# Kernel optimization log

Hardware: AMD Instinct MI355X
Metric: run time of the kernel (lower is better)

Reference implementation:

```python
import jax, jax.numpy as jnp
import numpy as np

B, T, D, H, DK, FF, V, L = 2, 1024, 768, 12, 64, 3072, 50257, 12


def setup_inputs() -> dict:
    key = jax.random.key(0)
    ks = jax.random.split(key, 9)
    s = 0.02  # matches nn.init.normal_(std=0.02)
    rn = lambda k, sh: jax.random.normal(k, sh, jnp.float32) * s
    return {
        "x": jax.random.randint(ks[0], (B, T), 0, V),
        "tok_emb": rn(ks[1], (V, D)),
        "pos_emb": rn(ks[2], (T, D)),
        "Wq": rn(ks[3], (L, D, D)), "bq": jnp.zeros((L, D), jnp.float32),
        "Wk": rn(ks[4], (L, D, D)), "bk": jnp.zeros((L, D), jnp.float32),
        "Wv": rn(ks[5], (L, D, D)), "bv": jnp.zeros((L, D), jnp.float32),
        "Wo": rn(ks[6], (L, D, D)), "bo": jnp.zeros((L, D), jnp.float32),
        "ln1_g": jnp.ones((L, D), jnp.float32), "ln1_b": jnp.zeros((L, D), jnp.float32),
        "ln2_g": jnp.ones((L, D), jnp.float32), "ln2_b": jnp.zeros((L, D), jnp.float32),
        "W1": rn(ks[7], (L, D, FF)), "b1": jnp.zeros((L, FF), jnp.float32),
        "W2": rn(ks[8], (L, FF, D)), "b2": jnp.zeros((L, D), jnp.float32),
        "lnf_g": jnp.ones((D,), jnp.float32), "lnf_b": jnp.zeros((D,), jnp.float32),
    }


def _ln(x, g, b, eps=1e-5):
    m = jnp.mean(x, axis=-1, keepdims=True)
    v = jnp.var(x, axis=-1, keepdims=True)  # biased var, like torch LayerNorm
    return (x - m) * jax.lax.rsqrt(v + eps) * g + b


def _forward(x, tok_emb, pos_emb, Wq, bq, Wk, bk, Wv, bv, Wo, bo,
             ln1_g, ln1_b, ln2_g, ln2_b, W1, b1, W2, b2, lnf_g, lnf_b):
    Bsz, Tn = x.shape
    h = tok_emb[x] + pos_emb[:Tn][None]  # [B,T,D]
    causal = jnp.tril(jnp.ones((Tn, Tn), dtype=bool))  # True = keep
    scale = 1.0 / np.sqrt(DK)

    def block(h, p):
        wq, bq_, wk, bk_, wv, bv_, wo, bo_, g1, be1, g2, be2, w1, bf1, w2, bf2 = p
        x2 = _ln(h, g1, be1)
        q = (x2 @ wq + bq_).reshape(Bsz, Tn, H, DK)
        k = (x2 @ wk + bk_).reshape(Bsz, Tn, H, DK)
        v = (x2 @ wv + bv_).reshape(Bsz, Tn, H, DK)
        scores = jnp.einsum("bqhd,bkhd->bhqk", q, k) * scale
        scores = jnp.where(causal, scores, -jnp.inf)
        attn = jax.nn.softmax(scores, axis=-1)  # dropout is identity in eval
        ctx = jnp.einsum("bhqk,bkhd->bqhd", attn, v).reshape(Bsz, Tn, D)
        h = h + ctx @ wo + bo_
        x2 = _ln(h, g2, be2)
        ff = jax.nn.gelu(x2 @ w1 + bf1, approximate=False) @ w2 + bf2  # exact GELU like F.gelu
        return h + ff, None

    params = (Wq, bq, Wk, bk, Wv, bv, Wo, bo, ln1_g, ln1_b, ln2_g, ln2_b, W1, b1, W2, b2)
    h, _ = jax.lax.scan(block, h, params)
    h = _ln(h, lnf_g, lnf_b)
    return h @ tok_emb.T  # tied lm_head, [B,T,V]


def reference(x, tok_emb, pos_emb, Wq, bq, Wk, bk, Wv, bv, Wo, bo,
              ln1_g, ln1_b, ln2_g, ln2_b, W1, b1, W2, b2, lnf_g, lnf_b):
    return _forward(x, tok_emb, pos_emb, Wq, bq, Wk, bk, Wv, bv, Wo, bo,
                    ln1_g, ln1_b, ln2_g, ln2_b, W1, b1, W2, b2, lnf_g, lnf_b)
```

## Files before the change

kernel.cpp:

```cpp
#include <hip/hip_runtime.h>
#include <cmath>

#define DI __device__ __forceinline__

typedef unsigned short u16;
typedef __bf16 bf16x8 __attribute__((ext_vector_type(8)));
typedef float f32x4 __attribute__((ext_vector_type(4)));

static constexpr int Bsz = 2, T = 1024, D = 768, H = 12, FF = 3072, V = 50257, L = 12;
static constexpr int M = Bsz * T;

DI u16 f2bf(float f) {
  unsigned u = __float_as_uint(f);
  u = (u + 0x7fffu + ((u >> 16) & 1u)) >> 16;
  return (u16)u;
}
DI float bf2f(u16 h) { return __uint_as_float(((unsigned)h) << 16); }

DI void gload_lds16(const void* g, void* l) {
  __builtin_amdgcn_global_load_lds((const __attribute__((address_space(1))) void*)g,
                                   (__attribute__((address_space(3))) void*)l, 16, 0, 0);
}

__launch_bounds__(256)
__global__ void transpose_cvt(const float* __restrict__ src, u16* __restrict__ dst, int R, int C) {
  __shared__ float tile[32][33];
  const int tx = threadIdx.x, ty = threadIdx.y;
  const int c0 = blockIdx.x * 32, r0 = blockIdx.y * 32;
  src += (size_t)blockIdx.z * R * C;
  dst += (size_t)blockIdx.z * R * C;
#pragma unroll
  for (int i = 0; i < 4; ++i)
    tile[ty + i * 8][tx] = src[(size_t)(r0 + ty + i * 8) * C + c0 + tx];
  __syncthreads();
#pragma unroll
  for (int i = 0; i < 4; ++i)
    dst[(size_t)(c0 + ty + i * 8) * R + r0 + tx] = f2bf(tile[tx][ty + i * 8]);
}

__global__ void convert_bf16(const float* __restrict__ src, u16* __restrict__ dst, long n4) {
  long i = (long)blockIdx.x * blockDim.x + threadIdx.x;
  long stride = (long)gridDim.x * blockDim.x;
  for (; i < n4; i += stride) {
    float4 f = ((const float4*)src)[i];
    ushort4 o;
    o.x = f2bf(f.x); o.y = f2bf(f.y); o.z = f2bf(f.z); o.w = f2bf(f.w);
    ((ushort4*)dst)[i] = o;
  }
}

__launch_bounds__(256)
__global__ void embed_kernel(const int* __restrict__ x, const float* __restrict__ tok,
                             const float* __restrict__ pos, float* __restrict__ h) {
  const int row = blockIdx.x, t = threadIdx.x;
  const int tt = row % T;
  const int id = x[row];
  float* o = h + (size_t)row * D;
  const float* te = tok + (size_t)id * D;
  const float* pe = pos + (size_t)tt * D;
  o[t] = te[t] + pe[t];
  o[t + 256] = te[t + 256] + pe[t + 256];
  o[t + 512] = te[t + 512] + pe[t + 512];
}

__launch_bounds__(256)
__global__ void layernorm_kernel(const float* __restrict__ in, const float* __restrict__ gw,
                                 const float* __restrict__ bw, u16* __restrict__ out) {
  const int row = blockIdx.x, t = threadIdx.x;
  const int lane = t & 63, wid = t >> 6;
  const float* x = in + (size_t)row * D;
  float v0 = x[t], v1 = x[t + 256], v2 = x[t + 512];
  float sum = v0 + v1 + v2;
  float sq = v0 * v0 + v1 * v1 + v2 * v2;
  for (int off = 1; off < 64; off <<= 1) {
    sum += __shfl_xor(sum, off);
    sq += __shfl_xor(sq, off);
  }
  __shared__ float ps[4], pq[4];
  if (lane == 0) { ps[wid] = sum; pq[wid] = sq; }
  __syncthreads();
  sum = ps[0] + ps[1] + ps[2] + ps[3];
  sq = pq[0] + pq[1] + pq[2] + pq[3];
  const float mean = sum * (1.0f / D);
  const float var = sq * (1.0f / D) - mean * mean;
  const float rstd = rsqrtf(var + 1e-5f);
  u16* o = out + (size_t)row * D;
  o[t] = f2bf((v0 - mean) * rstd * gw[t] + bw[t]);
  o[t + 256] = f2bf((v1 - mean) * rstd * gw[t + 256] + bw[t + 256]);
  o[t + 512] = f2bf((v2 - mean) * rstd * gw[t + 512] + bw[t + 512]);
}

template <int EPI, int BM, int BN, int BK>
DI void gemm_core(const u16* __restrict__ A, const u16* __restrict__ Bt,
                  const float* bias, float* outF, u16* outH, const float* resid,
                  int N, int K, int m0, int n0) {
  __shared__ u16 sA[BM * BK];
  __shared__ u16 sB[BN * BK];
  constexpr int FM = BM / 32, FN = BN / 32;
  constexpr int CPR = BK / 8;
  constexpr int KS = BK / 32;
  constexpr int AI = BM * BK / 8 / 256;
  constexpr int BI = BN * BK / 8 / 256;
  const int t = threadIdx.x;
  const int lane = t & 63, wid = t >> 6;

  f32x4 acc[FM][FN] = {};
  const int wr = (wid >> 1) * (BM / 2), wc = (wid & 1) * (BN / 2);
  const int rsel = lane & 15, ksel = lane >> 4;

  for (int k0 = 0; k0 < K; k0 += BK) {
#pragma unroll
    for (int i = 0; i < AI; ++i) {
      int c = t + i * 256;
      int row = c / CPR, ch = c % CPR;
      int g = ch ^ (row & (CPR - 1));
      gload_lds16(A + (size_t)(m0 + row) * K + k0 + g * 8, &sA[c * 8]);
    }
#pragma unroll
    for (int i = 0; i < BI; ++i) {
      int c = t + i * 256;
      int row = c / CPR, ch = c % CPR;
      int g = ch ^ (row & (CPR - 1));
      int nr = n0 + row;
      if (nr >= N) nr = N - 1;
      gload_lds16(Bt + (size_t)nr * K + k0 + g * 8, &sB[c * 8]);
    }
    __syncthreads();
#pragma unroll
    for (int ks = 0; ks < KS; ++ks) {
      bf16x8 af[FM], bfr[FN];
#pragma unroll
      for (int m = 0; m < FM; ++m) {
        int row = wr + m * 16 + rsel;
        int ch = (ksel + 4 * ks) ^ (row & (CPR - 1));
        af[m] = *(const bf16x8*)&sA[row * BK + ch * 8];
      }
#pragma unroll
      for (int n = 0; n < FN; ++n) {
        int row = wc + n * 16 + rsel;
        int ch = (ksel + 4 * ks) ^ (row & (CPR - 1));
        bfr[n] = *(const bf16x8*)&sB[row * BK + ch * 8];
      }
#pragma unroll
      for (int m = 0; m < FM; ++m)
#pragma unroll
        for (int n = 0; n < FN; ++n)
          acc[m][n] = __builtin_amdgcn_mfma_f32_16x16x32_bf16(af[m], bfr[n], acc[m][n], 0, 0, 0);
    }
    __syncthreads();
  }

  const int rq = lane >> 4;
#pragma unroll
  for (int m = 0; m < FM; ++m) {
#pragma unroll
    for (int n = 0; n < FN; ++n) {
      const int col = n0 + wc + n * 16 + rsel;
      if (col >= N) continue;
      const float bv = bias ? bias[col] : 0.0f;
#pragma unroll
      for (int i = 0; i < 4; ++i) {
        const int row = m0 + wr + m * 16 + rq * 4 + i;
        float v = acc[m][n][i] + bv;
        const size_t idx = (size_t)row * N + col;
        if (EPI == 0) {
          outH[idx] = f2bf(v);
        } else if (EPI == 1) {
          float ge = 0.5f * v * (1.0f + erff(v * 0.70710678118f));
          outH[idx] = f2bf(ge);
        } else if (EPI == 2) {
          outF[idx] = resid[idx] + v;
        } else {
          outF[idx] = v;
        }
      }
    }
  }
}

__launch_bounds__(256) __global__ void gemm_qkv(const u16* __restrict__ A, const u16* __restrict__ Bt,
                                                const float* b0, const float* b1, const float* b2,
                                                u16* out, long zsB, long zsOut) {
  const int z = blockIdx.z;
  gemm_core<0, 128, 128, 64>(A, Bt + (size_t)z * zsB, z == 0 ? b0 : (z == 1 ? b1 : b2),
                             nullptr, out + (size_t)z * zsOut, nullptr, D, D,
                             blockIdx.x * 128, blockIdx.y * 128);
}
__launch_bounds__(256) __global__ void gemm_proj(const u16* __restrict__ A, const u16* __restrict__ Bt,
                                                 const float* bias, float* h) {
  gemm_core<2, 64, 64, 64>(A, Bt, bias, h, nullptr, h, D, D, blockIdx.x * 64, blockIdx.y * 64);
}
__launch_bounds__(256) __global__ void gemm_ff1(const u16* __restrict__ A, const u16* __restrict__ Bt,
                                                const float* bias, u16* out) {
  gemm_core<1, 128, 128, 64>(A, Bt, bias, nullptr, out, nullptr, FF, D,
                             blockIdx.x * 128, blockIdx.y * 128);
}
__launch_bounds__(256) __global__ void gemm_ff2(const u16* __restrict__ A, const u16* __restrict__ Bt,
                                                const float* bias, float* h) {
  gemm_core<2, 64, 64, 64>(A, Bt, bias, h, nullptr, h, D, FF, blockIdx.x * 64, blockIdx.y * 64);
}
__launch_bounds__(256) __global__ void gemm_lm(const u16* __restrict__ A, const u16* __restrict__ Bt,
                                               float* out) {
  const int flat = blockIdx.y * gridDim.x + blockIdx.x;
  const int nwg = gridDim.x * gridDim.y;
  const int cpx = nwg >> 3;
  const int nf = (flat & 7) * cpx + (flat >> 3);
  const int m0 = (nf & 15) * 128, n0 = (nf >> 4) * 128;
  gemm_core<3, 128, 128, 64>(A, Bt, nullptr, out, nullptr, nullptr, V, D, m0, n0);
}

__launch_bounds__(256)
__global__ void attn_mfma(const u16* __restrict__ qbuf, const u16* __restrict__ kbuf,
                          const u16* __restrict__ vbuf, u16* __restrict__ ctx) {
  __shared__ u16 sK[64 * 64];
  __shared__ u16 sVT[64 * 72];
  __shared__ u16 sP[4][16 * 72];
  const int t = threadIdx.x, lane = t & 63, wid = t >> 6;
  const int l15 = lane & 15, g = lane >> 4;
  const int qc = gridDim.x - 1 - blockIdx.x;
  const int q0 = qc * 64;
  const int bh = blockIdx.y;
  const int b = bh / H, hh = bh % H;
  const size_t rowbase = (size_t)b * T;
  u16* sPw = &sP[wid][0];

  const size_t qoff = (rowbase + q0 + wid * 16 + l15) * D + hh * 64 + g * 8;
  bf16x8 aQ0 = *(const bf16x8*)&qbuf[qoff];
  bf16x8 aQ1 = *(const bf16x8*)&qbuf[qoff + 32];
#pragma unroll
  for (int j = 0; j < 8; ++j) {
    aQ0[j] = (__bf16)(0.125f * (float)aQ0[j]);
    aQ1[j] = (__bf16)(0.125f * (float)aQ1[j]);
  }

  float mr[4] = {-INFINITY, -INFINITY, -INFINITY, -INFINITY};
  float lr[4] = {0.f, 0.f, 0.f, 0.f};
  f32x4 o[4] = {};
  const int nt = qc + 1;

  for (int kt = 0; kt < nt; ++kt) {
    __syncthreads();
#pragma unroll
    for (int i = 0; i < 2; ++i) {
      int c = t + i * 256;
      int row = c >> 3, ch = c & 7;
      gload_lds16(kbuf + (rowbase + kt * 64 + row) * D + hh * 64 + (size_t)(ch ^ (row & 7)) * 8,
                  &sK[c * 8]);
    }
#pragma unroll
    for (int i = 0; i < 2; ++i) {
      int key = t & 63, d0 = (t >> 6) * 8 + i * 32;
      bf16x8 v8 = *(const bf16x8*)&vbuf[(rowbase + kt * 64 + key) * D + hh * 64 + d0];
#pragma unroll
      for (int j = 0; j < 8; ++j) sVT[(d0 + j) * 72 + key] = ((u16*)&v8)[j];
    }
    __syncthreads();

    f32x4 s[4];
#pragma unroll
    for (int f = 0; f < 4; ++f) {
      const int krow = f * 16 + l15;
      bf16x8 bk0 = *(const bf16x8*)&sK[krow * 64 + ((g ^ (krow & 7)) * 8)];
      bf16x8 bk1 = *(const bf16x8*)&sK[krow * 64 + (((g + 4) ^ (krow & 7)) * 8)];
      f32x4 z = {};
      z = __builtin_amdgcn_mfma_f32_16x16x32_bf16(aQ0, bk0, z, 0, 0, 0);
      s[f] = __builtin_amdgcn_mfma_f32_16x16x32_bf16(aQ1, bk1, z, 0, 0, 0);
    }

    float p[4][4], scl[4];
    const bool diag = (kt == qc);
#pragma unroll
    for (int i = 0; i < 4; ++i) {
      float v0 = s[0][i], v1 = s[1][i], v2 = s[2][i], v3 = s[3][i];
      if (diag) {
        const int qrow = q0 + wid * 16 + g * 4 + i;
        const int kb = kt * 64 + l15;
        v0 = (kb <= qrow) ? v0 : -INFINITY;
        v1 = (kb + 16 <= qrow) ? v1 : -INFINITY;
        v2 = (kb + 32 <= qrow) ? v2 : -INFINITY;
        v3 = (kb + 48 <= qrow) ? v3 : -INFINITY;
      }
      float mt = fmaxf(fmaxf(v0, v1), fmaxf(v2, v3));
#pragma unroll
      for (int off = 1; off < 16; off <<= 1) mt = fmaxf(mt, __shfl_xor(mt, off));
      const float mn = fmaxf(mr[i], mt);
      const float sc = __expf(mr[i] - mn);
      p[0][i] = __expf(v0 - mn); p[1][i] = __expf(v1 - mn);
      p[2][i] = __expf(v2 - mn); p[3][i] = __expf(v3 - mn);
      float rs = p[0][i] + p[1][i] + p[2][i] + p[3][i];
#pragma unroll
      for (int off = 1; off < 16; off <<= 1) rs += __shfl_xor(rs, off);
      lr[i] = lr[i] * sc + rs;
      mr[i] = mn;
      scl[i] = sc;
    }
#pragma unroll
    for (int n = 0; n < 4; ++n) {
      o[n][0] *= scl[0]; o[n][1] *= scl[1]; o[n][2] *= scl[2]; o[n][3] *= scl[3];
    }
#pragma unroll
    for (int f = 0; f < 4; ++f)
#pragma unroll
      for (int i = 0; i < 4; ++i)
        sPw[(g * 4 + i) * 72 + f * 16 + l15] = f2bf(p[f][i]);

#pragma unroll
    for (int kb = 0; kb < 2; ++kb) {
      bf16x8 pa = *(const bf16x8*)&sPw[l15 * 72 + kb * 32 + g * 8];
#pragma unroll
      for (int n = 0; n < 4; ++n) {
        bf16x8 bv = *(const bf16x8*)&sVT[(n * 16 + l15) * 72 + kb * 32 + g * 8];
        o[n] = __builtin_amdgcn_mfma_f32_16x16x32_bf16(pa, bv, o[n], 0, 0, 0);
      }
    }
  }

  float inv[4] = {1.0f / lr[0], 1.0f / lr[1], 1.0f / lr[2], 1.0f / lr[3]};
#pragma unroll
  for (int n = 0; n < 4; ++n)
#pragma unroll
    for (int i = 0; i < 4; ++i)
      ctx[(rowbase + q0 + wid * 16 + g * 4 + i) * D + hh * 64 + n * 16 + l15] =
          f2bf(o[n][i] * inv[i]);
}

extern "C" void kernel_launch(void* const* d_in, const int* in_sizes, int n_in,
                              void* d_out, int out_size, void* d_ws, size_t ws_size,
                              hipStream_t stream) {
  (void)in_sizes; (void)n_in; (void)out_size;
  const int* x = (const int*)d_in[0];
  const float* tok = (const float*)d_in[1];
  const float* pos = (const float*)d_in[2];
  const float* Wq = (const float*)d_in[3];
  const float* bq = (const float*)d_in[4];
  const float* Wk = (const float*)d_in[5];
  const float* bk = (const float*)d_in[6];
  const float* Wv = (const float*)d_in[7];
  const float* bv = (const float*)d_in[8];
  const float* Wo = (const float*)d_in[9];
  const float* bo = (const float*)d_in[10];
  const float* ln1_g = (const float*)d_in[11];
  const float* ln1_b = (const float*)d_in[12];
  const float* ln2_g = (const float*)d_in[13];
  const float* ln2_b = (const float*)d_in[14];
  const float* W1 = (const float*)d_in[15];
  const float* b1 = (const float*)d_in[16];
  const float* W2 = (const float*)d_in[17];
  const float* b2 = (const float*)d_in[18];
  const float* lnf_g = (const float*)d_in[19];
  const float* lnf_b = (const float*)d_in[20];

  char* ws = (char*)d_ws;
  size_t off = 0;
  auto alloc = [&](size_t bytes) {
    void* p = ws + off;
    off += (bytes + 255) & ~(size_t)255;
    return p;
  };
  u16* wqkvT = (u16*)alloc((size_t)3 * L * D * D * 2);
  u16* woT   = (u16*)alloc((size_t)L * D * D * 2);
  u16* w1T   = (u16*)alloc((size_t)L * D * FF * 2);
  u16* w2T   = (u16*)alloc((size_t)L * FF * D * 2);
  u16* tokT  = (u16*)alloc((size_t)V * D * 2);
  float* h   = (float*)alloc((size_t)M * D * 4);
  u16* x2    = (u16*)alloc((size_t)M * D * 2);
  u16* qkv   = (u16*)alloc((size_t)3 * M * D * 2);
  u16* ctx   = (u16*)alloc((size_t)M * D * 2);
  u16* ffb   = (u16*)alloc((size_t)M * FF * 2);
  u16* hf    = (u16*)alloc((size_t)M * D * 2);
  if (off > ws_size) return;

  const dim3 tb(32, 8);
  transpose_cvt<<<dim3(D / 32, D / 32, L), tb, 0, stream>>>(Wq, wqkvT + (size_t)0 * L * D * D, D, D);
  transpose_cvt<<<dim3(D / 32, D / 32, L), tb, 0, stream>>>(Wk, wqkvT + (size_t)1 * L * D * D, D, D);
  transpose_cvt<<<dim3(D / 32, D / 32, L), tb, 0, stream>>>(Wv, wqkvT + (size_t)2 * L * D * D, D, D);
  transpose_cvt<<<dim3(D / 32, D / 32, L), tb, 0, stream>>>(Wo, woT, D, D);
  transpose_cvt<<<dim3(FF / 32, D / 32, L), tb, 0, stream>>>(W1, w1T, D, FF);
  transpose_cvt<<<dim3(D / 32, FF / 32, L), tb, 0, stream>>>(W2, w2T, FF, D);
  convert_bf16<<<2048, 256, 0, stream>>>(tok, tokT, (long)V * D / 4);

  embed_kernel<<<M, 256, 0, stream>>>(x, tok, pos, h);

  for (int l = 0; l < L; ++l) {
    layernorm_kernel<<<M, 256, 0, stream>>>(h, ln1_g + (size_t)l * D, ln1_b + (size_t)l * D, x2);
    gemm_qkv<<<dim3(M / 128, D / 128, 3), 256, 0, stream>>>(
        x2, wqkvT + (size_t)l * D * D, bq + (size_t)l * D, bk + (size_t)l * D, bv + (size_t)l * D,
        qkv, (long)L * D * D, (long)M * D);
    attn_mfma<<<dim3(T / 64, Bsz * H), 256, 0, stream>>>(qkv, qkv + (size_t)M * D,
                                                         qkv + (size_t)2 * M * D, ctx);
    gemm_proj<<<dim3(M / 64, D / 64), 256, 0, stream>>>(ctx, woT + (size_t)l * D * D,
                                                        bo + (size_t)l * D, h);
    layernorm_kernel<<<M, 256, 0, stream>>>(h, ln2_g + (size_t)l * D, ln2_b + (size_t)l * D, x2);
    gemm_ff1<<<dim3(M / 128, FF / 128), 256, 0, stream>>>(x2, w1T + (size_t)l * D * FF,
                                                          b1 + (size_t)l * FF, ffb);
    gemm_ff2<<<dim3(M / 64, D / 64), 256, 0, stream>>>(ffb, w2T + (size_t)l * FF * D,
                                                       b2 + (size_t)l * D, h);
  }

  layernorm_kernel<<<M, 256, 0, stream>>>(h, lnf_g, lnf_b, hf);
  gemm_lm<<<dim3(M / 128, (V + 127) / 128), 256, 0, stream>>>(hf, tokT, (float*)d_out);
}
```

Baseline: 2.421 ms.

## Retile GEMMs, process 128 query rows per attention block, warp-per-row layernorm

Several independent changes land together. The four QKV/O weight transposes merge into one launch, and layernorm now gives each wavefront one row with float4 loads and no shared-memory reduction. The QKV GEMM tile shrinks to 64x64 for more blocks, and the FF1 and LM-head GEMMs use BK=32. Attention blocks now cover two 64-row query chunks so each K/V tile staged in shared memory is reused twice, at the cost of more registers and lower occupancy.

```diff
diff --git a/kernel.cpp b/kernel.cpp
--- a/kernel.cpp
+++ b/kernel.cpp
@@ -36,6 +36,27 @@
 #pragma unroll
   for (int i = 0; i < 4; ++i)
     dst[(size_t)(c0 + ty + i * 8) * R + r0 + tx] = f2bf(tile[tx][ty + i * 8]);
+}
+
+__launch_bounds__(256)
+__global__ void transpose_qkvo(const float* __restrict__ Wq, const float* __restrict__ Wk,
+                               const float* __restrict__ Wv, const float* __restrict__ Wo,
+                               u16* __restrict__ wqkvT, u16* __restrict__ woT) {
+  __shared__ float tile[32][33];
+  const int tx = threadIdx.x, ty = threadIdx.y;
+  const int c0 = blockIdx.x * 32, r0 = blockIdx.y * 32;
+  const int z = blockIdx.z, mat = z / L, layer = z % L;
+  const float* srcs[4] = {Wq, Wk, Wv, Wo};
+  const float* src = srcs[mat] + (size_t)layer * D * D;
+  u16* dst = (mat < 3) ? wqkvT + ((size_t)mat * L + layer) * D * D
+                       : woT + (size_t)layer * D * D;
+#pragma unroll
+  for (int i = 0; i < 4; ++i)
+    tile[ty + i * 8][tx] = src[(size_t)(r0 + ty + i * 8) * D + c0 + tx];
+  __syncthreads();
+#pragma unroll
+  for (int i = 0; i < 4; ++i)
+    dst[(size_t)(c0 + ty + i * 8) * D + r0 + tx] = f2bf(tile[tx][ty + i * 8]);
 }
 
 __global__ void convert_bf16(const float* __restrict__ src, u16* __restrict__ dst, long n4) {
@@ -66,28 +87,38 @@
 __launch_bounds__(256)
 __global__ void layernorm_kernel(const float* __restrict__ in, const float* __restrict__ gw,
                                  const float* __restrict__ bw, u16* __restrict__ out) {
-  const int row = blockIdx.x, t = threadIdx.x;
-  const int lane = t & 63, wid = t >> 6;
-  const float* x = in + (size_t)row * D;
-  float v0 = x[t], v1 = x[t + 256], v2 = x[t + 512];
-  float sum = v0 + v1 + v2;
-  float sq = v0 * v0 + v1 * v1 + v2 * v2;
+  const int lane = threadIdx.x & 63, wid = threadIdx.x >> 6;
+  const int row = blockIdx.x * 4 + wid;
+  const float4* x4 = (const float4*)(in + (size_t)row * D);
+  float4 v[3];
+  float sum = 0.f, sq = 0.f;
+#pragma unroll
+  for (int j = 0; j < 3; ++j) {
+    v[j] = x4[lane + 64 * j];
+    sum += v[j].x + v[j].y + v[j].z + v[j].w;
+    sq += v[j].x * v[j].x + v[j].y * v[j].y + v[j].z * v[j].z + v[j].w * v[j].w;
+  }
+#pragma unroll
   for (int off = 1; off < 64; off <<= 1) {
     sum += __shfl_xor(sum, off);
     sq += __shfl_xor(sq, off);
   }
-  __shared__ float ps[4], pq[4];
-  if (lane == 0) { ps[wid] = sum; pq[wid] = sq; }
-  __syncthreads();
-  sum = ps[0] + ps[1] + ps[2] + ps[3];
-  sq = pq[0] + pq[1] + pq[2] + pq[3];
   const float mean = sum * (1.0f / D);
   const float var = sq * (1.0f / D) - mean * mean;
   const float rstd = rsqrtf(var + 1e-5f);
-  u16* o = out + (size_t)row * D;
-  o[t] = f2bf((v0 - mean) * rstd * gw[t] + bw[t]);
-  o[t + 256] = f2bf((v1 - mean) * rstd * gw[t + 256] + bw[t + 256]);
-  o[t + 512] = f2bf((v2 - mean) * rstd * gw[t + 512] + bw[t + 512]);
+  const float4* g4 = (const float4*)gw;
+  const float4* b4 = (const float4*)bw;
+  ushort4* o4 = (ushort4*)(out + (size_t)row * D);
+#pragma unroll
+  for (int j = 0; j < 3; ++j) {
+    float4 g = g4[lane + 64 * j], b = b4[lane + 64 * j];
+    ushort4 o;
+    o.x = f2bf((v[j].x - mean) * rstd * g.x + b.x);
+    o.y = f2bf((v[j].y - mean) * rstd * g.y + b.y);
+    o.z = f2bf((v[j].z - mean) * rstd * g.z + b.z);
+    o.w = f2bf((v[j].w - mean) * rstd * g.w + b.w);
+    o4[lane + 64 * j] = o;
+  }
 }
 
 template <int EPI, int BM, int BN, int BK>
@@ -182,9 +213,9 @@
                                                 const float* b0, const float* b1, const float* b2,
                                                 u16* out, long zsB, long zsOut) {
   const int z = blockIdx.z;
-  gemm_core<0, 128, 128, 64>(A, Bt + (size_t)z * zsB, z == 0 ? b0 : (z == 1 ? b1 : b2),
-                             nullptr, out + (size_t)z * zsOut, nullptr, D, D,
-                             blockIdx.x * 128, blockIdx.y * 128);
+  gemm_core<0, 64, 64, 64>(A, Bt + (size_t)z * zsB, z == 0 ? b0 : (z == 1 ? b1 : b2),
+                           nullptr, out + (size_t)z * zsOut, nullptr, D, D,
+                           blockIdx.x * 64, blockIdx.y * 64);
 }
 __launch_bounds__(256) __global__ void gemm_proj(const u16* __restrict__ A, const u16* __restrict__ Bt,
                                                  const float* bias, float* h) {
@@ -192,7 +223,7 @@
 }
 __launch_bounds__(256) __global__ void gemm_ff1(const u16* __restrict__ A, const u16* __restrict__ Bt,
                                                 const float* bias, u16* out) {
-  gemm_core<1, 128, 128, 64>(A, Bt, bias, nullptr, out, nullptr, FF, D,
+  gemm_core<1, 128, 128, 32>(A, Bt, bias, nullptr, out, nullptr, FF, D,
                              blockIdx.x * 128, blockIdx.y * 128);
 }
 __launch_bounds__(256) __global__ void gemm_ff2(const u16* __restrict__ A, const u16* __restrict__ Bt,
@@ -206,7 +237,7 @@
   const int cpx = nwg >> 3;
   const int nf = (flat & 7) * cpx + (flat >> 3);
   const int m0 = (nf & 15) * 128, n0 = (nf >> 4) * 128;
-  gemm_core<3, 128, 128, 64>(A, Bt, nullptr, out, nullptr, nullptr, V, D, m0, n0);
+  gemm_core<3, 128, 128, 32>(A, Bt, nullptr, out, nullptr, nullptr, V, D, m0, n0);
 }
 
 __launch_bounds__(256)
@@ -214,29 +245,35 @@
                           const u16* __restrict__ vbuf, u16* __restrict__ ctx) {
   __shared__ u16 sK[64 * 64];
   __shared__ u16 sVT[64 * 72];
-  __shared__ u16 sP[4][16 * 72];
+  __shared__ u16 sP[4][32 * 72];
   const int t = threadIdx.x, lane = t & 63, wid = t >> 6;
   const int l15 = lane & 15, g = lane >> 4;
   const int qc = gridDim.x - 1 - blockIdx.x;
-  const int q0 = qc * 64;
+  const int q0 = qc * 128;
   const int bh = blockIdx.y;
   const int b = bh / H, hh = bh % H;
   const size_t rowbase = (size_t)b * T;
   u16* sPw = &sP[wid][0];
 
-  const size_t qoff = (rowbase + q0 + wid * 16 + l15) * D + hh * 64 + g * 8;
-  bf16x8 aQ0 = *(const bf16x8*)&qbuf[qoff];
-  bf16x8 aQ1 = *(const bf16x8*)&qbuf[qoff + 32];
+  const size_t qoffA = (rowbase + q0 + wid * 16 + l15) * D + hh * 64 + g * 8;
+  bf16x8 aQ0 = *(const bf16x8*)&qbuf[qoffA];
+  bf16x8 aQ1 = *(const bf16x8*)&qbuf[qoffA + 32];
+  bf16x8 bQ0 = *(const bf16x8*)&qbuf[qoffA + (size_t)64 * D];
+  bf16x8 bQ1 = *(const bf16x8*)&qbuf[qoffA + (size_t)64 * D + 32];
 #pragma unroll
   for (int j = 0; j < 8; ++j) {
     aQ0[j] = (__bf16)(0.125f * (float)aQ0[j]);
     aQ1[j] = (__bf16)(0.125f * (float)aQ1[j]);
-  }
-
-  float mr[4] = {-INFINITY, -INFINITY, -INFINITY, -INFINITY};
-  float lr[4] = {0.f, 0.f, 0.f, 0.f};
-  f32x4 o[4] = {};
-  const int nt = qc + 1;
+    bQ0[j] = (__bf16)(0.125f * (float)bQ0[j]);
+    bQ1[j] = (__bf16)(0.125f * (float)bQ1[j]);
+  }
+
+  float mrA[4] = {-INFINITY, -INFINITY, -INFINITY, -INFINITY};
+  float mrB[4] = {-INFINITY, -INFINITY, -INFINITY, -INFINITY};
+  float lrA[4] = {0.f, 0.f, 0.f, 0.f}, lrB[4] = {0.f, 0.f, 0.f, 0.f};
+  f32x4 oA[4] = {}, oB[4] = {};
+  const int nt = 2 * qc + 2;
+  const int lastA = 2 * qc;
 
   for (int kt = 0; kt < nt; ++kt) {
     __syncthreads();
@@ -256,72 +293,79 @@
     }
     __syncthreads();
 
-    f32x4 s[4];
-#pragma unroll
-    for (int f = 0; f < 4; ++f) {
-      const int krow = f * 16 + l15;
-      bf16x8 bk0 = *(const bf16x8*)&sK[krow * 64 + ((g ^ (krow & 7)) * 8)];
-      bf16x8 bk1 = *(const bf16x8*)&sK[krow * 64 + (((g + 4) ^ (krow & 7)) * 8)];
-      f32x4 z = {};
-      z = __builtin_amdgcn_mfma_f32_16x16x32_bf16(aQ0, bk0, z, 0, 0, 0);
-      s[f] = __builtin_amdgcn_mfma_f32_16x16x32_bf16(aQ1, bk1, z, 0, 0, 0);
-    }
-
-    float p[4][4], scl[4];
-    const bool diag = (kt == qc);
+    auto dofrag = [&](bf16x8 q0f, bf16x8 q1f, float* mr, float* lr, f32x4* o,
+                      int rowoff, bool diag) {
+      f32x4 s[4];
+#pragma unroll
+      for (int f = 0; f < 4; ++f) {
+        const int krow = f * 16 + l15;
+        bf16x8 bk0 = *(const bf16x8*)&sK[krow * 64 + ((g ^ (krow & 7)) * 8)];
+        bf16x8 bk1 = *(const bf16x8*)&sK[krow * 64 + (((g + 4) ^ (krow & 7)) * 8)];
+        f32x4 z = {};
+        z = __builtin_amdgcn_mfma_f32_16x16x32_bf16(q0f, bk0, z, 0, 0, 0);
+        s[f] = __builtin_amdgcn_mfma_f32_16x16x32_bf16(q1f, bk1, z, 0, 0, 0);
+      }
+      float p[4][4], scl[4];
+#pragma unroll
+      for (int i = 0; i < 4; ++i) {
+        float v0 = s[0][i], v1 = s[1][i], v2 = s[2][i], v3 = s[3][i];
+        if (diag) {
+          const int qrow = q0 + rowoff + wid * 16 + g * 4 + i;
+          const int kb = kt * 64 + l15;
+          v0 = (kb <= qrow) ? v0 : -INFINITY;
+          v1 = (kb + 16 <= qrow) ? v1 : -INFINITY;
+          v2 = (kb + 32 <= qrow) ? v2 : -INFINITY;
+          v3 = (kb + 48 <= qrow) ? v3 : -INFINITY;
+        }
+        float mt = fmaxf(fmaxf(v0, v1), fmaxf(v2, v3));
+#pragma unroll
+        for (int off = 1; off < 16; off <<= 1) mt = fmaxf(mt, __shfl_xor(mt, off));
+        const float mn = fmaxf(mr[i], mt);
+        const float sc = __expf(mr[i] - mn);
+        p[0][i] = __expf(v0 - mn); p[1][i] = __expf(v1 - mn);
+        p[2][i] = __expf(v2 - mn); p[3][i] = __expf(v3 - mn);
+        float rs = p[0][i] + p[1][i] + p[2][i] + p[3][i];
+#pragma unroll
+        for (int off = 1; off < 16; off <<= 1) rs += __shfl_xor(rs, off);
+        lr[i] = lr[i] * sc + rs;
+        mr[i] = mn;
+        scl[i] = sc;
+      }
+#pragma unroll
+      for (int n = 0; n < 4; ++n) {
+        o[n][0] *= scl[0]; o[n][1] *= scl[1]; o[n][2] *= scl[2]; o[n][3] *= scl[3];
+      }
+      u16* sPf = sPw + rowoff * (72 / 4);
+#pragma unroll
+      for (int f = 0; f < 4; ++f)
+#pragma unroll
+        for (int i = 0; i < 4; ++i)
+          sPf[(g * 4 + i) * 72 + f * 16 + l15] = f2bf(p[f][i]);
+#pragma unroll
+      for (int kb = 0; kb < 2; ++kb) {
+        bf16x8 pa = *(const bf16x8*)&sPf[l15 * 72 + kb * 32 + g * 8];
+#pragma unroll
+        for (int n = 0; n < 4; ++n) {
+          bf16x8 bv = *(const bf16x8*)&sVT[(n * 16 + l15) * 72 + kb * 32 + g * 8];
+          o[n] = __builtin_amdgcn_mfma_f32_16x16x32_bf16(pa, bv, o[n], 0, 0, 0);
+        }
+      }
+    };
+
+    if (kt <= lastA) dofrag(aQ0, aQ1, mrA, lrA, oA, 0, kt == lastA);
+    dofrag(bQ0, bQ1, mrB, lrB, oB, 64, kt == nt - 1);
+  }
+
+#pragma unroll
+  for (int i = 0; i < 4; ++i) { lrA[i] = 1.0f / lrA[i]; lrB[i] = 1.0f / lrB[i]; }
+#pragma unroll
+  for (int n = 0; n < 4; ++n)
 #pragma unroll
     for (int i = 0; i < 4; ++i) {
-      float v0 = s[0][i], v1 = s[1][i], v2 = s[2][i], v3 = s[3][i];
-      if (diag) {
-        const int qrow = q0 + wid * 16 + g * 4 + i;
-        const int kb = kt * 64 + l15;
-        v0 = (kb <= qrow) ? v0 : -INFINITY;
-        v1 = (kb + 16 <= qrow) ? v1 : -INFINITY;
-        v2 = (kb + 32 <= qrow) ? v2 : -INFINITY;
-        v3 = (kb + 48 <= qrow) ? v3 : -INFINITY;
-      }
-      float mt = fmaxf(fmaxf(v0, v1), fmaxf(v2, v3));
-#pragma unroll
-      for (int off = 1; off < 16; off <<= 1) mt = fmaxf(mt, __shfl_xor(mt, off));
-      const float mn = fmaxf(mr[i], mt);
-      const float sc = __expf(mr[i] - mn);
-      p[0][i] = __expf(v0 - mn); p[1][i] = __expf(v1 - mn);
-      p[2][i] = __expf(v2 - mn); p[3][i] = __expf(v3 - mn);
-      float rs = p[0][i] + p[1][i] + p[2][i] + p[3][i];
-#pragma unroll
-      for (int off = 1; off < 16; off <<= 1) rs += __shfl_xor(rs, off);
-      lr[i] = lr[i] * sc + rs;
-      mr[i] = mn;
-      scl[i] = sc;
-    }
-#pragma unroll
-    for (int n = 0; n < 4; ++n) {
-      o[n][0] *= scl[0]; o[n][1] *= scl[1]; o[n][2] *= scl[2]; o[n][3] *= scl[3];
-    }
-#pragma unroll
-    for (int f = 0; f < 4; ++f)
-#pragma unroll
-      for (int i = 0; i < 4; ++i)
-        sPw[(g * 4 + i) * 72 + f * 16 + l15] = f2bf(p[f][i]);
-
-#pragma unroll
-    for (int kb = 0; kb < 2; ++kb) {
-      bf16x8 pa = *(const bf16x8*)&sPw[l15 * 72 + kb * 32 + g * 8];
-#pragma unroll
-      for (int n = 0; n < 4; ++n) {
-        bf16x8 bv = *(const bf16x8*)&sVT[(n * 16 + l15) * 72 + kb * 32 + g * 8];
-        o[n] = __builtin_amdgcn_mfma_f32_16x16x32_bf16(pa, bv, o[n], 0, 0, 0);
-      }
-    }
-  }
-
-  float inv[4] = {1.0f / lr[0], 1.0f / lr[1], 1.0f / lr[2], 1.0f / lr[3]};
-#pragma unroll
-  for (int n = 0; n < 4; ++n)
-#pragma unroll
-    for (int i = 0; i < 4; ++i)
-      ctx[(rowbase + q0 + wid * 16 + g * 4 + i) * D + hh * 64 + n * 16 + l15] =
-          f2bf(o[n][i] * inv[i]);
+      const size_t base = (rowbase + q0 + wid * 16 + g * 4 + i) * D + hh * 64 + n * 16 + l15;
+      ctx[base] = f2bf(oA[n][i] * lrA[i]);
+      ctx[base + (size_t)64 * D] = f2bf(oB[n][i] * lrB[i]);
+    }
 }
 
 extern "C" void kernel_launch(void* const* d_in, const int* in_sizes, int n_in,
@@ -371,10 +415,7 @@
   if (off > ws_size) return;
 
   const dim3 tb(32, 8);
-  transpose_cvt<<<dim3(D / 32, D / 32, L), tb, 0, stream>>>(Wq, wqkvT + (size_t)0 * L * D * D, D, D);
-  transpose_cvt<<<dim3(D / 32, D / 32, L), tb, 0, stream>>>(Wk, wqkvT + (size_t)1 * L * D * D, D, D);
-  transpose_cvt<<<dim3(D / 32, D / 32, L), tb, 0, stream>>>(Wv, wqkvT + (size_t)2 * L * D * D, D, D);
-  transpose_cvt<<<dim3(D / 32, D / 32, L), tb, 0, stream>>>(Wo, woT, D, D);
+  transpose_qkvo<<<dim3(D / 32, D / 32, 4 * L), tb, 0, stream>>>(Wq, Wk, Wv, Wo, wqkvT, woT);
   transpose_cvt<<<dim3(FF / 32, D / 32, L), tb, 0, stream>>>(W1, w1T, D, FF);
   transpose_cvt<<<dim3(D / 32, FF / 32, L), tb, 0, stream>>>(W2, w2T, FF, D);
   convert_bf16<<<2048, 256, 0, stream>>>(tok, tokT, (long)V * D / 4);
@@ -382,21 +423,21 @@
   embed_kernel<<<M, 256, 0, stream>>>(x, tok, pos, h);
 
   for (int l = 0; l < L; ++l) {
-    layernorm_kernel<<<M, 256, 0, stream>>>(h, ln1_g + (size_t)l * D, ln1_b + (size_t)l * D, x2);
-    gemm_qkv<<<dim3(M / 128, D / 128, 3), 256, 0, stream>>>(
+    layernorm_kernel<<<M / 4, 256, 0, stream>>>(h, ln1_g + (size_t)l * D, ln1_b + (size_t)l * D, x2);
+    gemm_qkv<<<dim3(M / 64, D / 64, 3), 256, 0, stream>>>(
         x2, wqkvT + (size_t)l * D * D, bq + (size_t)l * D, bk + (size_t)l * D, bv + (size_t)l * D,
         qkv, (long)L * D * D, (long)M * D);
-    attn_mfma<<<dim3(T / 64, Bsz * H), 256, 0, stream>>>(qkv, qkv + (size_t)M * D,
-                                                         qkv + (size_t)2 * M * D, ctx);
+    attn_mfma<<<dim3(T / 128, Bsz * H), 256, 0, stream>>>(qkv, qkv + (size_t)M * D,
+                                                          qkv + (size_t)2 * M * D, ctx);
     gemm_proj<<<dim3(M / 64, D / 64), 256, 0, stream>>>(ctx, woT + (size_t)l * D * D,
                                                         bo + (size_t)l * D, h);
-    layernorm_kernel<<<M, 256, 0, stream>>>(h, ln2_g + (size_t)l * D, ln2_b + (size_t)l * D, x2);
+    layernorm_kernel<<<M / 4, 256, 0, stream>>>(h, ln2_g + (size_t)l * D, ln2_b + (size_t)l * D, x2);
     gemm_ff1<<<dim3(M / 128, FF / 128), 256, 0, stream>>>(x2, w1T + (size_t)l * D * FF,
                                                           b1 + (size_t)l * FF, ffb);
     gemm_ff2<<<dim3(M / 64, D / 64), 256, 0, stream>>>(ffb, w2T + (size_t)l * FF * D,
                                                        b2 + (size_t)l * D, h);
   }
 
-  layernorm_kernel<<<M, 256, 0, stream>>>(h, lnf_g, lnf_b, hf);
+  layernorm_kernel<<<M / 4, 256, 0, stream>>>(h, lnf_g, lnf_b, hf);
   gemm_lm<<<dim3(M / 128, (V + 127) / 128), 256, 0, stream>>>(hf, tokT, (float*)d_out);
 }
```

Result: slower. 2.625 ms (+8.4%).
